# Performance work log

Hardware: AMD Instinct MI355X
Metric: run time of the kernel (lower is better)

The kernel has to match this reference:

```python
import jax, jax.numpy as jnp
import numpy as np

N = 50000      # nodes
E = 800000     # edges
D = 128        # node_dim
H = 4          # heads
C = 64         # hidden_dim per head
B = 64         # graphs in batch
OUT = 10       # output_dim
SLOPE = 0.2    # GATConv leaky_relu negative slope (PyG default)


def gat_conv(x, src, dst, W, a_src, a_dst, bias, concat):
    """One PyG-style GATConv layer. src/dst already include self-loops."""
    n = x.shape[0]
    h = (x @ W).reshape(n, H, C)                       # [N,H,C]
    al_s = jnp.sum(h * a_src, axis=-1)                  # [N,H]
    al_d = jnp.sum(h * a_dst, axis=-1)                  # [N,H]
    e = jax.nn.leaky_relu(al_s[src] + al_d[dst], SLOPE)  # [E+N,H]
    m = jax.ops.segment_max(e, dst, num_segments=n)      # per-target-node max
    e = jnp.exp(e - m[dst])
    den = jax.ops.segment_sum(e, dst, num_segments=n)
    alpha = e / (den[dst] + 1e-16)                       # [E+N,H]
    msg = h[src] * alpha[:, :, None]                     # [E+N,H,C]
    out = jax.ops.segment_sum(msg, dst, num_segments=n)  # [N,H,C]
    out = out.reshape(n, H * C) if concat else out.mean(axis=1)
    return out + bias


def gat_forward(x, edge_index, batch, W0, b0, as0, ad0, W1, b1, as1, ad1,
                W2, b2, as2, ad2, pW1, pb1, pW2, pb2):
    n = x.shape[0]
    loop = jnp.arange(n, dtype=edge_index.dtype)
    src = jnp.concatenate([edge_index[0], loop])
    dst = jnp.concatenate([edge_index[1], loop])

    h = gat_conv(x, src, dst, W0, as0, ad0, b0, concat=True)
    h = jax.nn.elu(h)                                    # dropout = identity (eval)
    h = gat_conv(h, src, dst, W1, as1, ad1, b1, concat=True)
    h = jax.nn.elu(h)
    h = gat_conv(h, src, dst, W2, as2, ad2, b2, concat=False)  # [N,C]

    # global_mean_pool
    sums = jax.ops.segment_sum(h, batch, num_segments=B)        # [B,C]
    cnt = jax.ops.segment_sum(jnp.ones((n,), h.dtype), batch, num_segments=B)
    pooled = sums / jnp.maximum(cnt, 1.0)[:, None]

    # predictor MLP
    z = jax.nn.relu(pooled @ pW1 + pb1)
    return z @ pW2 + pb2                                        # [B,OUT]


def setup_inputs() -> dict:
    key = jax.random.key(0)
    ks = jax.random.split(key, 24)
    gl = lambda k, shp, fan: (jax.random.normal(k, shp, jnp.float32) / np.float32(np.sqrt(fan)))
    x = jax.random.normal(ks[0], (N, D), jnp.float32)
    edge_index = jax.random.randint(ks[1], (2, E), 0, N, dtype=jnp.int32)
    batch = jnp.sort(jax.random.randint(ks[2], (N,), 0, B, dtype=jnp.int32))
    return dict(
        x=x, edge_index=edge_index, batch=batch,
        W0=gl(ks[3], (D, H * C), D), b0=jnp.zeros((H * C,), jnp.float32),
        as0=gl(ks[4], (H, C), C), ad0=gl(ks[5], (H, C), C),
        W1=gl(ks[6], (H * C, H * C), H * C), b1=jnp.zeros((H * C,), jnp.float32),
        as1=gl(ks[7], (H, C), C), ad1=gl(ks[8], (H, C), C),
        W2=gl(ks[9], (H * C, H * C), H * C), b2=jnp.zeros((C,), jnp.float32),
        as2=gl(ks[10], (H, C), C), ad2=gl(ks[11], (H, C), C),
        pW1=gl(ks[12], (C, C // 2), C), pb1=jnp.zeros((C // 2,), jnp.float32),
        pW2=gl(ks[13], (C // 2, OUT), C // 2), pb2=jnp.zeros((OUT,), jnp.float32),
    )


def reference(x, edge_index, batch, W0, b0, as0, ad0, W1, b1, as1, ad1,
              W2, b2, as2, ad2, pW1, pb1, pW2, pb2):
    return gat_forward(x, edge_index, batch, W0, b0, as0, ad0, W1, b1, as1, ad1,
                       W2, b2, as2, ad2, pW1, pb1, pW2, pb2)
```

## Files before the change

### kernel.cpp

```cpp
#include <hip/hip_runtime.h>
#include <hip/hip_fp16.h>
#include <cstdint>

#define N_NODES 50000
#define E_EDGES 800000
#define HC 256
#define B_GR 64
#define OUT_DIM 10
#define SLOPE 0.2f
#define NBLK_SCAN ((N_NODES + 255) / 256)

using f16x8 = __attribute__((ext_vector_type(8))) _Float16;
using f32x4 = __attribute__((ext_vector_type(4))) float;

__global__ void wsplit_kernel(const float* __restrict__ W, _Float16* __restrict__ wt_hi,
                              _Float16* __restrict__ wt_lo, int K) {
    int i = blockIdx.x * 256 + threadIdx.x;
    if (i >= K * 256) return;
    int k = i >> 8, n = i & 255;
    float v = W[i];
    _Float16 h = (_Float16)v;
    _Float16 l = (_Float16)(v - (float)h);
    int oidx = ((((k >> 5) * 256 + n) * 4) + ((k >> 3) & 3)) * 8 + (k & 7);
    wt_hi[oidx] = h;
    wt_lo[oidx] = l;
}

template<int K>
__global__ __launch_bounds__(256) void gemm_mfma(const float* __restrict__ A,
        const _Float16* __restrict__ wt_hi, const _Float16* __restrict__ wt_lo,
        __half* __restrict__ h_half,
        const float* __restrict__ a_src, const float* __restrict__ a_dst,
        float* __restrict__ al_s, float* __restrict__ al_d, int M) {
    __shared__ _Float16 a_hi[64][64];
    __shared__ _Float16 a_lo[64][64];
    int tid = threadIdx.x;
    int w = tid >> 6;
    int l = tid & 63;
    int rr = l & 15;
    int kg = l >> 4;
    int row0 = blockIdx.x * 64;
    int lrow = tid >> 2;
    int lgp  = (tid & 3) * 2;

    f32x4 acc[4][4] = {};

    for (int k0 = 0; k0 < K; k0 += 64) {
        if (k0 > 0) __syncthreads();
        int gr = row0 + lrow;
#pragma unroll
        for (int gi = 0; gi < 2; ++gi) {
            int g = lgp + gi;
            float vv[8];
            if (gr < M) {
                float4 p = *(const float4*)&A[(size_t)gr * K + k0 + g * 8];
                float4 q = *(const float4*)&A[(size_t)gr * K + k0 + g * 8 + 4];
                vv[0] = p.x; vv[1] = p.y; vv[2] = p.z; vv[3] = p.w;
                vv[4] = q.x; vv[5] = q.y; vv[6] = q.z; vv[7] = q.w;
            } else {
#pragma unroll
                for (int j = 0; j < 8; ++j) vv[j] = 0.f;
            }
            f16x8 vh, vl;
#pragma unroll
            for (int j = 0; j < 8; ++j) {
                _Float16 hh = (_Float16)vv[j];
                vh[j] = hh;
                vl[j] = (_Float16)(vv[j] - (float)hh);
            }
            int gs = g ^ (lrow & 7);
            *(f16x8*)&a_hi[lrow][gs * 8] = vh;
            *(f16x8*)&a_lo[lrow][gs * 8] = vl;
        }
        __syncthreads();
#pragma unroll
        for (int c = 0; c < 2; ++c) {
            f16x8 ah[4], alo[4];
#pragma unroll
            for (int fm = 0; fm < 4; ++fm) {
                int row = fm * 16 + rr;
                int gsw = ((c * 4 + kg) ^ (row & 7));
                ah[fm]  = *(const f16x8*)&a_hi[row][gsw * 8];
                alo[fm] = *(const f16x8*)&a_lo[row][gsw * 8];
            }
            int chunk = (k0 >> 5) + c;
#pragma unroll
            for (int fn = 0; fn < 4; ++fn) {
                int col = w * 64 + fn * 16 + rr;
                size_t boff = (((size_t)chunk * 256 + col) * 4 + kg) * 8;
                f16x8 bh = *(const f16x8*)&wt_hi[boff];
                f16x8 bl = *(const f16x8*)&wt_lo[boff];
#pragma unroll
                for (int fm = 0; fm < 4; ++fm) {
                    acc[fm][fn] = __builtin_amdgcn_mfma_f32_16x16x32_f16(ah[fm],  bh, acc[fm][fn], 0, 0, 0);
                    acc[fm][fn] = __builtin_amdgcn_mfma_f32_16x16x32_f16(ah[fm],  bl, acc[fm][fn], 0, 0, 0);
                    acc[fm][fn] = __builtin_amdgcn_mfma_f32_16x16x32_f16(alo[fm], bh, acc[fm][fn], 0, 0, 0);
                }
            }
        }
    }

    int head = w;
    float asv[4], adv[4];
#pragma unroll
    for (int fn = 0; fn < 4; ++fn) {
        asv[fn] = a_src[head * 64 + fn * 16 + rr];
        adv[fn] = a_dst[head * 64 + fn * 16 + rr];
    }
#pragma unroll
    for (int fm = 0; fm < 4; ++fm) {
#pragma unroll
        for (int r = 0; r < 4; ++r) {
            int row = fm * 16 + kg * 4 + r;
            int gr = row0 + row;
            float ps = acc[fm][0][r] * asv[0] + acc[fm][1][r] * asv[1]
                     + acc[fm][2][r] * asv[2] + acc[fm][3][r] * asv[3];
            float pd = acc[fm][0][r] * adv[0] + acc[fm][1][r] * adv[1]
                     + acc[fm][2][r] * adv[2] + acc[fm][3][r] * adv[3];
#pragma unroll
            for (int off = 1; off < 16; off <<= 1) {
                ps += __shfl_xor(ps, off, 64);
                pd += __shfl_xor(pd, off, 64);
            }
            if (gr < M) {
#pragma unroll
                for (int fn = 0; fn < 4; ++fn)
                    h_half[(size_t)gr * HC + w * 64 + fn * 16 + rr] = __float2half(acc[fm][fn][r]);
                if (rr == 0) {
                    al_s[gr * 4 + head] = ps;
                    al_d[gr * 4 + head] = pd;
                }
            }
        }
    }
}

__global__ void init_cnt(int* cnt) {
    int i = blockIdx.x * blockDim.x + threadIdx.x;
    if (i < N_NODES) cnt[i] = 1;
}
__global__ void hist_kernel(const int* __restrict__ dsts, int* cnt) {
    int i = blockIdx.x * blockDim.x + threadIdx.x;
    if (i < E_EDGES) atomicAdd(&cnt[dsts[i]], 1);
}
__global__ __launch_bounds__(256) void scan_bsum(const int* __restrict__ cnt,
                                                 int* __restrict__ bsum) {
    __shared__ int ws[4];
    int t = threadIdx.x;
    int i = blockIdx.x * 256 + t;
    int v = (i < N_NODES) ? cnt[i] : 0;
#pragma unroll
    for (int off = 1; off < 64; off <<= 1) v += __shfl_xor(v, off, 64);
    if ((t & 63) == 0) ws[t >> 6] = v;
    __syncthreads();
    if (t == 0) bsum[blockIdx.x] = ws[0] + ws[1] + ws[2] + ws[3];
}
__global__ __launch_bounds__(256) void scan_boff(const int* __restrict__ bsum,
                                                 int* __restrict__ boff) {
    __shared__ int s[256];
    int t = threadIdx.x;
    int v = (t < NBLK_SCAN) ? bsum[t] : 0;
    s[t] = v;
    __syncthreads();
    for (int off = 1; off < 256; off <<= 1) {
        int u = (t >= off) ? s[t - off] : 0;
        __syncthreads();
        s[t] += u;
        __syncthreads();
    }
    if (t < NBLK_SCAN) boff[t] = s[t] - v;
}
__global__ __launch_bounds__(256) void scan_final(const int* __restrict__ cnt,
        const int* __restrict__ boff, int* __restrict__ row_ptr,
        int* __restrict__ cursor) {
    __shared__ int s[256];
    int b = blockIdx.x, t = threadIdx.x;
    int i = b * 256 + t;
    int v = (i < N_NODES) ? cnt[i] : 0;
    s[t] = v;
    __syncthreads();
    for (int off = 1; off < 256; off <<= 1) {
        int u = (t >= off) ? s[t - off] : 0;
        __syncthreads();
        s[t] += u;
        __syncthreads();
    }
    int rp = boff[b] + s[t] - v;
    if (i < N_NODES) { row_ptr[i] = rp; cursor[i] = rp; }
    if (i == N_NODES - 1) row_ptr[N_NODES] = rp + v;
}
__global__ void scatter_kernel(const int* __restrict__ srcs, const int* __restrict__ dsts,
                               int* cursor, int* col) {
    int i = blockIdx.x * blockDim.x + threadIdx.x;
    if (i >= E_EDGES + N_NODES) return;
    int s, d;
    if (i < E_EDGES) { s = srcs[i]; d = dsts[i]; }
    else             { s = d = i - E_EDGES; }
    int pos = atomicAdd(&cursor[d], 1);
    col[pos] = s;
}

__global__ __launch_bounds__(256) void agg_kernel(const __half* __restrict__ hh,
        const float* __restrict__ al_s, const float* __restrict__ al_d,
        const int* __restrict__ row_ptr, const int* __restrict__ col,
        const float* __restrict__ bias, float* __restrict__ out, int mode) {
    __shared__ int   lds_col[4][64];
    __shared__ float lds_alpha[4][64][4];
    int wid  = threadIdx.x >> 6;
    int lane = threadIdx.x & 63;
    int hf   = lane >> 5;
    int ln   = lane & 31;
    int nodeA = blockIdx.x * 8 + wid * 2;
    int nodeB = nodeA + 1;
    int sA = row_ptr[nodeA], eA = row_ptr[nodeA + 1];
    int sB = row_ptr[nodeB], eB = row_ptr[nodeB + 1];
    int degA = eA - sA, degB = eB - sB;

    if (degA <= 32 && degB <= 32) {
        int node  = hf ? nodeB : nodeA;
        int start = hf ? sB : sA;
        int deg   = hf ? degB : degA;
        int degmax = max(degA, degB);
        const float4 ald = *(const float4*)&al_d[node * 4];
        bool active = ln < deg;
        int s = active ? col[start + ln] : 0;
        float4 as = *(const float4*)&al_s[s * 4];
        float e0 = as.x + ald.x; e0 = e0 > 0.f ? e0 : SLOPE * e0;
        float e1 = as.y + ald.y; e1 = e1 > 0.f ? e1 : SLOPE * e1;
        float e2 = as.z + ald.z; e2 = e2 > 0.f ? e2 : SLOPE * e2;
        float e3 = as.w + ald.w; e3 = e3 > 0.f ? e3 : SLOPE * e3;
        float m0 = active ? e0 : -1e30f, m1 = active ? e1 : -1e30f;
        float m2 = active ? e2 : -1e30f, m3 = active ? e3 : -1e30f;
#pragma unroll
        for (int off = 1; off < 32; off <<= 1) {
            m0 = fmaxf(m0, __shfl_xor(m0, off, 64));
            m1 = fmaxf(m1, __shfl_xor(m1, off, 64));
            m2 = fmaxf(m2, __shfl_xor(m2, off, 64));
            m3 = fmaxf(m3, __shfl_xor(m3, off, 64));
        }
        float x0 = active ? expf(e0 - m0) : 0.f;
        float x1 = active ? expf(e1 - m1) : 0.f;
        float x2 = active ? expf(e2 - m2) : 0.f;
        float x3 = active ? expf(e3 - m3) : 0.f;
        float d0 = x0, d1 = x1, d2 = x2, d3 = x3;
#pragma unroll
        for (int off = 1; off < 32; off <<= 1) {
            d0 += __shfl_xor(d0, off, 64);
            d1 += __shfl_xor(d1, off, 64);
            d2 += __shfl_xor(d2, off, 64);
            d3 += __shfl_xor(d3, off, 64);
        }
        float4 a4;
        a4.x = x0 / (d0 + 1e-16f); a4.y = x1 / (d1 + 1e-16f);
        a4.z = x2 / (d2 + 1e-16f); a4.w = x3 / (d3 + 1e-16f);
        int e = hf * 32 + ln;
        lds_col[wid][e] = s;
        *(float4*)&lds_alpha[wid][e][0] = a4;
        int head = ln >> 3;
        int ch0 = ln * 8;
        float acc[8] = {0.f, 0.f, 0.f, 0.f, 0.f, 0.f, 0.f, 0.f};
        int ebase = hf * 32;
        for (int t0 = 0; t0 < degmax; t0 += 4) {
            float wv[4]; float4 raw[4];
#pragma unroll
            for (int k = 0; k < 4; ++k) {
                int t = t0 + k;
                int tt = min(t, deg - 1);
                int s2 = lds_col[wid][ebase + tt];
                wv[k] = (t < deg) ? lds_alpha[wid][ebase + tt][head] : 0.f;
                raw[k] = *(const float4*)&hh[(size_t)s2 * HC + ch0];
            }
#pragma unroll
            for (int k = 0; k < 4; ++k) {
                const __half2* hp = (const __half2*)&raw[k];
                float2 f0 = __half22float2(hp[0]);
                float2 f1 = __half22float2(hp[1]);
                float2 f2 = __half22float2(hp[2]);
                float2 f3 = __half22float2(hp[3]);
                acc[0] = fmaf(wv[k], f0.x, acc[0]); acc[1] = fmaf(wv[k], f0.y, acc[1]);
                acc[2] = fmaf(wv[k], f1.x, acc[2]); acc[3] = fmaf(wv[k], f1.y, acc[3]);
                acc[4] = fmaf(wv[k], f2.x, acc[4]); acc[5] = fmaf(wv[k], f2.y, acc[5]);
                acc[6] = fmaf(wv[k], f3.x, acc[6]); acc[7] = fmaf(wv[k], f3.y, acc[7]);
            }
        }
        if (mode == 0) {
            float b8[8];
            *(float4*)&b8[0] = *(const float4*)&bias[ch0];
            *(float4*)&b8[4] = *(const float4*)&bias[ch0 + 4];
            float v[8];
#pragma unroll
            for (int j = 0; j < 8; ++j) {
                float t = acc[j] + b8[j];
                v[j] = t > 0.f ? t : expm1f(t);
            }
            *(float4*)&out[(size_t)node * HC + ch0]     = *(float4*)&v[0];
            *(float4*)&out[(size_t)node * HC + ch0 + 4] = *(float4*)&v[4];
        } else {
#pragma unroll
            for (int j = 0; j < 8; ++j) {
                acc[j] += __shfl_xor(acc[j], 8, 64);
                acc[j] += __shfl_xor(acc[j], 16, 64);
            }
            if (ln < 8) {
                float v[8];
#pragma unroll
                for (int j = 0; j < 8; ++j)
                    v[j] = acc[j] * 0.25f + bias[ln * 8 + j];
                *(float4*)&out[(size_t)node * 64 + ln * 8]     = *(float4*)&v[0];
                *(float4*)&out[(size_t)node * 64 + ln * 8 + 4] = *(float4*)&v[4];
            }
        }
        return;
    }

    for (int nn = 0; nn < 2; ++nn) {
        int node = nodeA + nn;
        int start = row_ptr[node], end = row_ptr[node + 1];
        int deg = end - start;
        const float4 ald = *(const float4*)&al_d[node * 4];
        int head = lane >> 4;
        float ald_h = head == 0 ? ald.x : head == 1 ? ald.y : head == 2 ? ald.z : ald.w;
        float ax = 0.f, ay = 0.f, az = 0.f, aw = 0.f;

        if (deg <= 64) {
            int j = start + lane;
            bool active = j < end;
            int s = active ? col[j] : 0;
            float4 as = *(const float4*)&al_s[s * 4];
            float e0 = as.x + ald.x; e0 = e0 > 0.f ? e0 : SLOPE * e0;
            float e1 = as.y + ald.y; e1 = e1 > 0.f ? e1 : SLOPE * e1;
            float e2 = as.z + ald.z; e2 = e2 > 0.f ? e2 : SLOPE * e2;
            float e3 = as.w + ald.w; e3 = e3 > 0.f ? e3 : SLOPE * e3;
            float m0 = active ? e0 : -1e30f, m1 = active ? e1 : -1e30f;
            float m2 = active ? e2 : -1e30f, m3 = active ? e3 : -1e30f;
#pragma unroll
            for (int off = 1; off < 64; off <<= 1) {
                m0 = fmaxf(m0, __shfl_xor(m0, off, 64));
                m1 = fmaxf(m1, __shfl_xor(m1, off, 64));
                m2 = fmaxf(m2, __shfl_xor(m2, off, 64));
                m3 = fmaxf(m3, __shfl_xor(m3, off, 64));
            }
            float x0 = active ? expf(e0 - m0) : 0.f;
            float x1 = active ? expf(e1 - m1) : 0.f;
            float x2 = active ? expf(e2 - m2) : 0.f;
            float x3 = active ? expf(e3 - m3) : 0.f;
            float d0 = x0, d1 = x1, d2 = x2, d3 = x3;
#pragma unroll
            for (int off = 1; off < 64; off <<= 1) {
                d0 += __shfl_xor(d0, off, 64);
                d1 += __shfl_xor(d1, off, 64);
                d2 += __shfl_xor(d2, off, 64);
                d3 += __shfl_xor(d3, off, 64);
            }
            float4 a4;
            a4.x = x0 / (d0 + 1e-16f); a4.y = x1 / (d1 + 1e-16f);
            a4.z = x2 / (d2 + 1e-16f); a4.w = x3 / (d3 + 1e-16f);
            lds_col[wid][lane] = s;
            *(float4*)&lds_alpha[wid][lane][0] = a4;
            for (int t0 = 0; t0 < deg; t0 += 8) {
                int nr = deg - t0;
                float wv[8]; float2 raw[8];
#pragma unroll
                for (int k = 0; k < 8; ++k) {
                    if (k < nr) {
                        int s2 = lds_col[wid][t0 + k];
                        wv[k] = lds_alpha[wid][t0 + k][head];
                        raw[k] = *(const float2*)&hh[(size_t)s2 * HC + lane * 4];
                    } else {
                        wv[k] = 0.f;
                        raw[k] = make_float2(0.f, 0.f);
                    }
                }
#pragma unroll
                for (int k = 0; k < 8; ++k) {
                    float2 f0 = __half22float2(*(__half2*)&raw[k].x);
                    float2 f1 = __half22float2(*(__half2*)&raw[k].y);
                    ax = fmaf(wv[k], f0.x, ax); ay = fmaf(wv[k], f0.y, ay);
                    az = fmaf(wv[k], f1.x, az); aw = fmaf(wv[k], f1.y, aw);
                }
            }
        } else {
            float m0 = -1e30f, m1 = -1e30f, m2 = -1e30f, m3 = -1e30f;
            for (int j = start + lane; j < end; j += 64) {
                int s = col[j];
                float4 as = *(const float4*)&al_s[s * 4];
                float e0 = as.x + ald.x; e0 = e0 > 0.f ? e0 : SLOPE * e0;
                float e1 = as.y + ald.y; e1 = e1 > 0.f ? e1 : SLOPE * e1;
                float e2 = as.z + ald.z; e2 = e2 > 0.f ? e2 : SLOPE * e2;
                float e3 = as.w + ald.w; e3 = e3 > 0.f ? e3 : SLOPE * e3;
                m0 = fmaxf(m0, e0); m1 = fmaxf(m1, e1);
                m2 = fmaxf(m2, e2); m3 = fmaxf(m3, e3);
            }
#pragma unroll
            for (int off = 1; off < 64; off <<= 1) {
                m0 = fmaxf(m0, __shfl_xor(m0, off, 64));
                m1 = fmaxf(m1, __shfl_xor(m1, off, 64));
                m2 = fmaxf(m2, __shfl_xor(m2, off, 64));
                m3 = fmaxf(m3, __shfl_xor(m3, off, 64));
            }
            float d0 = 0.f, d1 = 0.f, d2 = 0.f, d3 = 0.f;
            for (int j = start + lane; j < end; j += 64) {
                int s = col[j];
                float4 as = *(const float4*)&al_s[s * 4];
                float e0 = as.x + ald.x; e0 = e0 > 0.f ? e0 : SLOPE * e0;
                float e1 = as.y + ald.y; e1 = e1 > 0.f ? e1 : SLOPE * e1;
                float e2 = as.z + ald.z; e2 = e2 > 0.f ? e2 : SLOPE * e2;
                float e3 = as.w + ald.w; e3 = e3 > 0.f ? e3 : SLOPE * e3;
                d0 += expf(e0 - m0); d1 += expf(e1 - m1);
                d2 += expf(e2 - m2); d3 += expf(e3 - m3);
            }
#pragma unroll
            for (int off = 1; off < 64; off <<= 1) {
                d0 += __shfl_xor(d0, off, 64);
                d1 += __shfl_xor(d1, off, 64);
                d2 += __shfl_xor(d2, off, 64);
                d3 += __shfl_xor(d3, off, 64);
            }
            float inv0 = 1.f / (d0 + 1e-16f), inv1 = 1.f / (d1 + 1e-16f);
            float inv2 = 1.f / (d2 + 1e-16f), inv3 = 1.f / (d3 + 1e-16f);
            float m_h   = head == 0 ? m0   : head == 1 ? m1   : head == 2 ? m2   : m3;
            float inv_h = head == 0 ? inv0 : head == 1 ? inv1 : head == 2 ? inv2 : inv3;
            for (int jb = start; jb < end; jb += 64) {
                int j = jb + lane;
                int cs = (j < end) ? col[j] : 0;
                int cnt2 = min(64, end - jb);
                for (int t = 0; t < cnt2; ++t) {
                    int s = __shfl(cs, t, 64);
                    float als2 = al_s[s * 4 + head];
                    float e = als2 + ald_h; e = e > 0.f ? e : SLOPE * e;
                    float wv = expf(e - m_h) * inv_h;
                    float2 raw = *(const float2*)&hh[(size_t)s * HC + lane * 4];
                    float2 f0 = __half22float2(*(__half2*)&raw.x);
                    float2 f1 = __half22float2(*(__half2*)&raw.y);
                    ax = fmaf(wv, f0.x, ax); ay = fmaf(wv, f0.y, ay);
                    az = fmaf(wv, f1.x, az); aw = fmaf(wv, f1.y, aw);
                }
            }
        }

        if (mode == 0) {
            float4 b4 = *(const float4*)&bias[lane * 4];
            float vx = ax + b4.x; vx = vx > 0.f ? vx : expm1f(vx);
            float vy = ay + b4.y; vy = vy > 0.f ? vy : expm1f(vy);
            float vz = az + b4.z; vz = vz > 0.f ? vz : expm1f(vz);
            float vw = aw + b4.w; vw = vw > 0.f ? vw : expm1f(vw);
            float4 v = make_float4(vx, vy, vz, vw);
            *(float4*)&out[(size_t)node * HC + lane * 4] = v;
        } else {
#pragma unroll
            for (int off = 16; off < 64; off <<= 1) {
                ax += __shfl_xor(ax, off, 64);
                ay += __shfl_xor(ay, off, 64);
                az += __shfl_xor(az, off, 64);
                aw += __shfl_xor(aw, off, 64);
            }
            if (lane < 16) {
                float4 b4 = *(const float4*)&bias[lane * 4];
                float4 v = make_float4(ax * 0.25f + b4.x, ay * 0.25f + b4.y,
                                       az * 0.25f + b4.z, aw * 0.25f + b4.w);
                *(float4*)&out[(size_t)node * 64 + lane * 4] = v;
            }
        }
    }
}

__global__ void pool_zero(float* __restrict__ pooled) {
    int i = blockIdx.x * blockDim.x + threadIdx.x;
    if (i < B_GR * 64) pooled[i] = 0.f;
}

__global__ __launch_bounds__(256) void pool_kernel(const float* __restrict__ act,
        const int* __restrict__ batch, float* __restrict__ pooled) {
    int b = blockIdx.x;
    int chunk = blockIdx.y;
    int warp = threadIdx.x >> 6;
    int lane = threadIdx.x & 63;
    int lo = 0, hi = N_NODES;
    while (lo < hi) { int mid = (lo + hi) >> 1; if (batch[mid] < b) lo = mid + 1; else hi = mid; }
    int s = lo;
    lo = 0; hi = N_NODES;
    while (lo < hi) { int mid = (lo + hi) >> 1; if (batch[mid] < b + 1) lo = mid + 1; else hi = mid; }
    int e = lo;
    float sum = 0.f;
    for (int n = s + chunk * 4 + warp; n < e; n += 64)
        sum += act[(size_t)n * 64 + lane];
    atomicAdd(&pooled[b * 64 + lane], sum);
}

__global__ __launch_bounds__(64) void mlp_kernel(const float* __restrict__ pooled,
        const int* __restrict__ batch,
        const float* __restrict__ pW1, const float* __restrict__ pb1,
        const float* __restrict__ pW2, const float* __restrict__ pb2,
        float* __restrict__ outp) {
    __shared__ float p[64];
    __shared__ float z[32];
    int b = blockIdx.x, t = threadIdx.x;
    int lo = 0, hi = N_NODES;
    while (lo < hi) { int mid = (lo + hi) >> 1; if (batch[mid] < b) lo = mid + 1; else hi = mid; }
    int s = lo;
    lo = 0; hi = N_NODES;
    while (lo < hi) { int mid = (lo + hi) >> 1; if (batch[mid] < b + 1) lo = mid + 1; else hi = mid; }
    int e = lo;
    float inv = 1.f / (float)max(e - s, 1);
    p[t] = pooled[b * 64 + t] * inv;
    __syncthreads();
    if (t < 32) {
        float s2 = pb1[t];
        for (int c = 0; c < 64; ++c) s2 += p[c] * pW1[c * 32 + t];
        z[t] = s2 > 0.f ? s2 : 0.f;
    }
    __syncthreads();
    if (t < OUT_DIM) {
        float s2 = pb2[t];
        for (int k = 0; k < 32; ++k) s2 += z[k] * pW2[k * 10 + t];
        outp[b * 10 + t] = s2;
    }
}

extern "C" void kernel_launch(void* const* d_in, const int* in_sizes, int n_in,
                              void* d_out, int out_size, void* d_ws, size_t ws_size,
                              hipStream_t stream) {
    const float* x    = (const float*)d_in[0];
    const int*   ei   = (const int*)d_in[1];
    const int*   batch= (const int*)d_in[2];
    const float* W0   = (const float*)d_in[3];
    const float* b0   = (const float*)d_in[4];
    const float* as0  = (const float*)d_in[5];
    const float* ad0  = (const float*)d_in[6];
    const float* W1   = (const float*)d_in[7];
    const float* b1   = (const float*)d_in[8];
    const float* as1  = (const float*)d_in[9];
    const float* ad1  = (const float*)d_in[10];
    const float* W2   = (const float*)d_in[11];
    const float* b2   = (const float*)d_in[12];
    const float* as2  = (const float*)d_in[13];
    const float* ad2  = (const float*)d_in[14];
    const float* pW1  = (const float*)d_in[15];
    const float* pb1  = (const float*)d_in[16];
    const float* pW2  = (const float*)d_in[17];
    const float* pb2  = (const float*)d_in[18];
    float* out = (float*)d_out;

    char* ws = (char*)d_ws;
    size_t off = 0;
    auto alloc = [&](size_t bytes) -> void* {
        void* p = ws + off;
        off += (bytes + 255) & ~(size_t)255;
        return p;
    };
    __half* h_half = (__half*)alloc((size_t)N_NODES * HC * 2);
    float* act    = (float*)alloc((size_t)N_NODES * HC * 4);
    float* als    = (float*)alloc((size_t)N_NODES * 4 * 4);
    float* ald    = (float*)alloc((size_t)N_NODES * 4 * 4);
    int*   cnt    = (int*)alloc((size_t)N_NODES * 4);
    int*   row_ptr= (int*)alloc((size_t)(N_NODES + 1) * 4);
    int*   cursor = (int*)alloc((size_t)N_NODES * 4);
    int*   col    = (int*)alloc((size_t)(E_EDGES + N_NODES) * 4);
    float* pooled = (float*)alloc((size_t)B_GR * 64 * 4);
    int*   bsum   = (int*)alloc((size_t)NBLK_SCAN * 4);
    int*   boff   = (int*)alloc((size_t)NBLK_SCAN * 4);
    _Float16* w0h = (_Float16*)alloc((size_t)128 * 256 * 2);
    _Float16* w0l = (_Float16*)alloc((size_t)128 * 256 * 2);
    _Float16* w1h = (_Float16*)alloc((size_t)256 * 256 * 2);
    _Float16* w1l = (_Float16*)alloc((size_t)256 * 256 * 2);
    _Float16* w2h = (_Float16*)alloc((size_t)256 * 256 * 2);
    _Float16* w2l = (_Float16*)alloc((size_t)256 * 256 * 2);

    const int* srcs = ei;
    const int* dsts = ei + E_EDGES;

    wsplit_kernel<<<(128 * 256 + 255) / 256, 256, 0, stream>>>(W0, w0h, w0l, 128);
    wsplit_kernel<<<(256 * 256 + 255) / 256, 256, 0, stream>>>(W1, w1h, w1l, 256);
    wsplit_kernel<<<(256 * 256 + 255) / 256, 256, 0, stream>>>(W2, w2h, w2l, 256);

    init_cnt<<<(N_NODES + 255) / 256, 256, 0, stream>>>(cnt);
    hist_kernel<<<(E_EDGES + 255) / 256, 256, 0, stream>>>(dsts, cnt);
    scan_bsum<<<NBLK_SCAN, 256, 0, stream>>>(cnt, bsum);
    scan_boff<<<1, 256, 0, stream>>>(bsum, boff);
    scan_final<<<NBLK_SCAN, 256, 0, stream>>>(cnt, boff, row_ptr, cursor);
    scatter_kernel<<<(E_EDGES + N_NODES + 255) / 256, 256, 0, stream>>>(srcs, dsts, cursor, col);

    int gblk = (N_NODES + 63) / 64;
    int nblk = (N_NODES + 7) / 8;

    gemm_mfma<128><<<gblk, 256, 0, stream>>>(x, w0h, w0l, h_half, as0, ad0, als, ald, N_NODES);
    agg_kernel<<<nblk, 256, 0, stream>>>(h_half, als, ald, row_ptr, col, b0, act, 0);
    gemm_mfma<256><<<gblk, 256, 0, stream>>>(act, w1h, w1l, h_half, as1, ad1, als, ald, N_NODES);
    agg_kernel<<<nblk, 256, 0, stream>>>(h_half, als, ald, row_ptr, col, b1, act, 0);
    gemm_mfma<256><<<gblk, 256, 0, stream>>>(act, w2h, w2l, h_half, as2, ad2, als, ald, N_NODES);
    agg_kernel<<<nblk, 256, 0, stream>>>(h_half, als, ald, row_ptr, col, b2, act, 1);

    pool_zero<<<(B_GR * 64 + 255) / 256, 256, 0, stream>>>(pooled);
    dim3 pgrid(B_GR, 16);
    pool_kernel<<<pgrid, 256, 0, stream>>>(act, batch, pooled);
    mlp_kernel<<<B_GR, 64, 0, stream>>>(pooled, batch, pW1, pb1, pW2, pb2, out);
}
```

Baseline: 445.0 us.

## Store hidden activations in fp16, pre-split x, double-buffer GEMM A tiles via LDS loads

The hidden-layer activations written by aggregation are now stored as fp16, so layers 1 and 2 read half the bytes and drop the lo-term MFMA (two terms instead of three). The input x is split into hi/lo fp16 in one fused prep kernel that also splits all three weight matrices. The GEMM now stages A tiles with global_load_lds into a double buffer, overlapping the next tile's load with the current tile's compute. Pooling uses one 1024-thread block per graph with an LDS reduction instead of atomics and a zeroing kernel. Rounding activations to fp16 and dropping the lo term lowers GEMM input precision and may affect accuracy.

Result: faster. 423.1 us (-4.9%).

```diff
diff --git a/kernel.cpp b/kernel.cpp
--- a/kernel.cpp
+++ b/kernel.cpp
@@ -13,77 +13,96 @@
 using f16x8 = __attribute__((ext_vector_type(8))) _Float16;
 using f32x4 = __attribute__((ext_vector_type(4))) float;
 
-__global__ void wsplit_kernel(const float* __restrict__ W, _Float16* __restrict__ wt_hi,
-                              _Float16* __restrict__ wt_lo, int K) {
-    int i = blockIdx.x * 256 + threadIdx.x;
-    if (i >= K * 256) return;
+#define GLOAD_LDS16(gsrc, ldst) \
+    __builtin_amdgcn_global_load_lds((const __attribute__((address_space(1))) void*)(gsrc), \
+        (__attribute__((address_space(3))) void*)(ldst), 16, 0, 0)
+
+__device__ inline void wsplit_one(const float* W, _Float16* wh, _Float16* wl,
+                                  int K, int i) {
     int k = i >> 8, n = i & 255;
     float v = W[i];
     _Float16 h = (_Float16)v;
     _Float16 l = (_Float16)(v - (float)h);
     int oidx = ((((k >> 5) * 256 + n) * 4) + ((k >> 3) & 3)) * 8 + (k & 7);
-    wt_hi[oidx] = h;
-    wt_lo[oidx] = l;
-}
-
-template<int K>
-__global__ __launch_bounds__(256) void gemm_mfma(const float* __restrict__ A,
+    wh[oidx] = h;
+    wl[oidx] = l;
+}
+
+__global__ void prep_split(const float* __restrict__ x,
+        _Float16* __restrict__ xhi, _Float16* __restrict__ xlo,
+        const float* __restrict__ W0, _Float16* __restrict__ w0h, _Float16* __restrict__ w0l,
+        const float* __restrict__ W1, _Float16* __restrict__ w1h, _Float16* __restrict__ w1l,
+        const float* __restrict__ W2, _Float16* __restrict__ w2h, _Float16* __restrict__ w2l) {
+    const int NX = N_NODES * 128;
+    int i = blockIdx.x * 256 + threadIdx.x;
+    if (i < NX) {
+        float v = x[i];
+        _Float16 h = (_Float16)v;
+        xhi[i] = h;
+        xlo[i] = (_Float16)(v - (float)h);
+        return;
+    }
+    int j = i - NX;
+    if (j < 128 * 256) { wsplit_one(W0, w0h, w0l, 128, j); return; }
+    j -= 128 * 256;
+    if (j < 256 * 256) { wsplit_one(W1, w1h, w1l, 256, j); return; }
+    j -= 256 * 256;
+    if (j < 256 * 256) { wsplit_one(W2, w2h, w2l, 256, j); return; }
+}
+
+template<int K, int TERMS>
+__global__ __launch_bounds__(256) void gemm16(const _Float16* __restrict__ Ahi,
+        const _Float16* __restrict__ Alo,
         const _Float16* __restrict__ wt_hi, const _Float16* __restrict__ wt_lo,
         __half* __restrict__ h_half,
         const float* __restrict__ a_src, const float* __restrict__ a_dst,
         float* __restrict__ al_s, float* __restrict__ al_d, int M) {
-    __shared__ _Float16 a_hi[64][64];
-    __shared__ _Float16 a_lo[64][64];
+    __shared__ _Float16 abuf[2][2][64][64];
     int tid = threadIdx.x;
     int w = tid >> 6;
     int l = tid & 63;
     int rr = l & 15;
     int kg = l >> 4;
     int row0 = blockIdx.x * 64;
-    int lrow = tid >> 2;
-    int lgp  = (tid & 3) * 2;
+    int srow = tid >> 3;
+    int sgs  = tid & 7;
 
     f32x4 acc[4][4] = {};
-
-    for (int k0 = 0; k0 < K; k0 += 64) {
-        if (k0 > 0) __syncthreads();
-        int gr = row0 + lrow;
-#pragma unroll
-        for (int gi = 0; gi < 2; ++gi) {
-            int g = lgp + gi;
-            float vv[8];
-            if (gr < M) {
-                float4 p = *(const float4*)&A[(size_t)gr * K + k0 + g * 8];
-                float4 q = *(const float4*)&A[(size_t)gr * K + k0 + g * 8 + 4];
-                vv[0] = p.x; vv[1] = p.y; vv[2] = p.z; vv[3] = p.w;
-                vv[4] = q.x; vv[5] = q.y; vv[6] = q.z; vv[7] = q.w;
-            } else {
-#pragma unroll
-                for (int j = 0; j < 8; ++j) vv[j] = 0.f;
-            }
-            f16x8 vh, vl;
-#pragma unroll
-            for (int j = 0; j < 8; ++j) {
-                _Float16 hh = (_Float16)vv[j];
-                vh[j] = hh;
-                vl[j] = (_Float16)(vv[j] - (float)hh);
-            }
-            int gs = g ^ (lrow & 7);
-            *(f16x8*)&a_hi[lrow][gs * 8] = vh;
-            *(f16x8*)&a_lo[lrow][gs * 8] = vl;
-        }
-        __syncthreads();
+    const int NT = K / 64;
+
+    auto stage = [&](int buf, int t) {
+        int k0 = t * 64;
+#pragma unroll
+        for (int i = 0; i < 2; ++i) {
+            int row = i * 32 + srow;
+            int g = sgs ^ (row & 7);
+            int gr = min(row0 + row, M - 1);
+            char* dst = (char*)abuf + buf * 16384 + i * 4096 + w * 1024;
+            GLOAD_LDS16(&Ahi[(size_t)gr * K + k0 + g * 8], dst);
+            if constexpr (TERMS == 3)
+                GLOAD_LDS16(&Alo[(size_t)gr * K + k0 + g * 8], dst + 8192);
+        }
+    };
+
+    stage(0, 0);
+    __syncthreads();
+    int cur = 0;
+    for (int t = 0; t < NT; ++t) {
+        if (t + 1 < NT) stage(cur ^ 1, t + 1);
+        const _Float16* base_hi = &abuf[cur][0][0][0];
+        const _Float16* base_lo = &abuf[cur][1][0][0];
 #pragma unroll
         for (int c = 0; c < 2; ++c) {
-            f16x8 ah[4], alo[4];
+            f16x8 ah[4], alo_[4];
 #pragma unroll
             for (int fm = 0; fm < 4; ++fm) {
                 int row = fm * 16 + rr;
                 int gsw = ((c * 4 + kg) ^ (row & 7));
-                ah[fm]  = *(const f16x8*)&a_hi[row][gsw * 8];
-                alo[fm] = *(const f16x8*)&a_lo[row][gsw * 8];
-            }
-            int chunk = (k0 >> 5) + c;
+                ah[fm] = *(const f16x8*)&base_hi[row * 64 + gsw * 8];
+                if constexpr (TERMS == 3)
+                    alo_[fm] = *(const f16x8*)&base_lo[row * 64 + gsw * 8];
+            }
+            int chunk = t * 2 + c;
 #pragma unroll
             for (int fn = 0; fn < 4; ++fn) {
                 int col = w * 64 + fn * 16 + rr;
@@ -92,12 +111,15 @@
                 f16x8 bl = *(const f16x8*)&wt_lo[boff];
 #pragma unroll
                 for (int fm = 0; fm < 4; ++fm) {
-                    acc[fm][fn] = __builtin_amdgcn_mfma_f32_16x16x32_f16(ah[fm],  bh, acc[fm][fn], 0, 0, 0);
-                    acc[fm][fn] = __builtin_amdgcn_mfma_f32_16x16x32_f16(ah[fm],  bl, acc[fm][fn], 0, 0, 0);
-                    acc[fm][fn] = __builtin_amdgcn_mfma_f32_16x16x32_f16(alo[fm], bh, acc[fm][fn], 0, 0, 0);
+                    acc[fm][fn] = __builtin_amdgcn_mfma_f32_16x16x32_f16(ah[fm], bh, acc[fm][fn], 0, 0, 0);
+                    acc[fm][fn] = __builtin_amdgcn_mfma_f32_16x16x32_f16(ah[fm], bl, acc[fm][fn], 0, 0, 0);
+                    if constexpr (TERMS == 3)
+                        acc[fm][fn] = __builtin_amdgcn_mfma_f32_16x16x32_f16(alo_[fm], bh, acc[fm][fn], 0, 0, 0);
                 }
             }
         }
+        __syncthreads();
+        cur ^= 1;
     }
 
     int head = w;
@@ -203,7 +225,8 @@
 __global__ __launch_bounds__(256) void agg_kernel(const __half* __restrict__ hh,
         const float* __restrict__ al_s, const float* __restrict__ al_d,
         const int* __restrict__ row_ptr, const int* __restrict__ col,
-        const float* __restrict__ bias, float* __restrict__ out, int mode) {
+        const float* __restrict__ bias, _Float16* __restrict__ out_h,
+        float* __restrict__ out_f, int mode) {
     __shared__ int   lds_col[4][64];
     __shared__ float lds_alpha[4][64][4];
     int wid  = threadIdx.x >> 6;
@@ -287,14 +310,13 @@
             float b8[8];
             *(float4*)&b8[0] = *(const float4*)&bias[ch0];
             *(float4*)&b8[4] = *(const float4*)&bias[ch0 + 4];
-            float v[8];
+            _Float16 v[8];
 #pragma unroll
             for (int j = 0; j < 8; ++j) {
                 float t = acc[j] + b8[j];
-                v[j] = t > 0.f ? t : expm1f(t);
-            }
-            *(float4*)&out[(size_t)node * HC + ch0]     = *(float4*)&v[0];
-            *(float4*)&out[(size_t)node * HC + ch0 + 4] = *(float4*)&v[4];
+                v[j] = (_Float16)(t > 0.f ? t : expm1f(t));
+            }
+            *(float4*)&out_h[(size_t)node * HC + ch0] = *(float4*)v;
         } else {
 #pragma unroll
             for (int j = 0; j < 8; ++j) {
@@ -306,8 +328,8 @@
 #pragma unroll
                 for (int j = 0; j < 8; ++j)
                     v[j] = acc[j] * 0.25f + bias[ln * 8 + j];
-                *(float4*)&out[(size_t)node * 64 + ln * 8]     = *(float4*)&v[0];
-                *(float4*)&out[(size_t)node * 64 + ln * 8 + 4] = *(float4*)&v[4];
+                *(float4*)&out_f[(size_t)node * 64 + ln * 8]     = *(float4*)&v[0];
+                *(float4*)&out_f[(size_t)node * 64 + ln * 8 + 4] = *(float4*)&v[4];
             }
         }
         return;
@@ -444,8 +466,8 @@
             float vy = ay + b4.y; vy = vy > 0.f ? vy : expm1f(vy);
             float vz = az + b4.z; vz = vz > 0.f ? vz : expm1f(vz);
             float vw = aw + b4.w; vw = vw > 0.f ? vw : expm1f(vw);
-            float4 v = make_float4(vx, vy, vz, vw);
-            *(float4*)&out[(size_t)node * HC + lane * 4] = v;
+            _Float16 v[4] = {(_Float16)vx, (_Float16)vy, (_Float16)vz, (_Float16)vw};
+            *(float2*)&out_h[(size_t)node * HC + lane * 4] = *(float2*)v;
         } else {
 #pragma unroll
             for (int off = 16; off < 64; off <<= 1) {
@@ -458,21 +480,16 @@
                 float4 b4 = *(const float4*)&bias[lane * 4];
                 float4 v = make_float4(ax * 0.25f + b4.x, ay * 0.25f + b4.y,
                                        az * 0.25f + b4.z, aw * 0.25f + b4.w);
-                *(float4*)&out[(size_t)node * 64 + lane * 4] = v;
-            }
-        }
-    }
-}
-
-__global__ void pool_zero(float* __restrict__ pooled) {
-    int i = blockIdx.x * blockDim.x + threadIdx.x;
-    if (i < B_GR * 64) pooled[i] = 0.f;
-}
-
-__global__ __launch_bounds__(256) void pool_kernel(const float* __restrict__ act,
+                *(float4*)&out_f[(size_t)node * 64 + lane * 4] = v;
+            }
+        }
+    }
+}
+
+__global__ __launch_bounds__(1024) void pool_kernel(const float* __restrict__ act,
         const int* __restrict__ batch, float* __restrict__ pooled) {
+    __shared__ float part[16][64];
     int b = blockIdx.x;
-    int chunk = blockIdx.y;
     int warp = threadIdx.x >> 6;
     int lane = threadIdx.x & 63;
     int lo = 0, hi = N_NODES;
@@ -482,9 +499,16 @@
     while (lo < hi) { int mid = (lo + hi) >> 1; if (batch[mid] < b + 1) lo = mid + 1; else hi = mid; }
     int e = lo;
     float sum = 0.f;
-    for (int n = s + chunk * 4 + warp; n < e; n += 64)
+    for (int n = s + warp; n < e; n += 16)
         sum += act[(size_t)n * 64 + lane];
-    atomicAdd(&pooled[b * 64 + lane], sum);
+    part[warp][lane] = sum;
+    __syncthreads();
+    if (threadIdx.x < 64) {
+        float t = 0.f;
+#pragma unroll
+        for (int r = 0; r < 16; ++r) t += part[r][lane];
+        pooled[b * 64 + lane] = t;
+    }
 }
 
 __global__ __launch_bounds__(64) void mlp_kernel(const float* __restrict__ pooled,
@@ -548,8 +572,11 @@
         off += (bytes + 255) & ~(size_t)255;
         return p;
     };
-    __half* h_half = (__half*)alloc((size_t)N_NODES * HC * 2);
-    float* act    = (float*)alloc((size_t)N_NODES * HC * 4);
+    __half*    h_half = (__half*)alloc((size_t)N_NODES * HC * 2);
+    _Float16*  act_h  = (_Float16*)alloc((size_t)N_NODES * HC * 2);
+    float*     act_f  = (float*)alloc((size_t)N_NODES * 64 * 4);
+    _Float16*  xhi    = (_Float16*)alloc((size_t)N_NODES * 128 * 2);
+    _Float16*  xlo    = (_Float16*)alloc((size_t)N_NODES * 128 * 2);
     float* als    = (float*)alloc((size_t)N_NODES * 4 * 4);
     float* ald    = (float*)alloc((size_t)N_NODES * 4 * 4);
     int*   cnt    = (int*)alloc((size_t)N_NODES * 4);
@@ -569,9 +596,9 @@
     const int* srcs = ei;
     const int* dsts = ei + E_EDGES;
 
-    wsplit_kernel<<<(128 * 256 + 255) / 256, 256, 0, stream>>>(W0, w0h, w0l, 128);
-    wsplit_kernel<<<(256 * 256 + 255) / 256, 256, 0, stream>>>(W1, w1h, w1l, 256);
-    wsplit_kernel<<<(256 * 256 + 255) / 256, 256, 0, stream>>>(W2, w2h, w2l, 256);
+    const int PREP_N = N_NODES * 128 + 128 * 256 + 256 * 256 + 256 * 256;
+    prep_split<<<(PREP_N + 255) / 256, 256, 0, stream>>>(
+        x, xhi, xlo, W0, w0h, w0l, W1, w1h, w1l, W2, w2h, w2l);
 
     init_cnt<<<(N_NODES + 255) / 256, 256, 0, stream>>>(cnt);
     hist_kernel<<<(E_EDGES + 255) / 256, 256, 0, stream>>>(dsts, cnt);
@@ -583,15 +610,13 @@
     int gblk = (N_NODES + 63) / 64;
     int nblk = (N_NODES + 7) / 8;
 
-    gemm_mfma<128><<<gblk, 256, 0, stream>>>(x, w0h, w0l, h_half, as0, ad0, als, ald, N_NODES);
-    agg_kernel<<<nblk, 256, 0, stream>>>(h_half, als, ald, row_ptr, col, b0, act, 0);
-    gemm_mfma<256><<<gblk, 256, 0, stream>>>(act, w1h, w1l, h_half, as1, ad1, als, ald, N_NODES);
-    agg_kernel<<<nblk, 256, 0, stream>>>(h_half, als, ald, row_ptr, col, b1, act, 0);
-    gemm_mfma<256><<<gblk, 256, 0, stream>>>(act, w2h, w2l, h_half, as2, ad2, als, ald, N_NODES);
-    agg_kernel<<<nblk, 256, 0, stream>>>(h_half, als, ald, row_ptr, col, b2, act, 1);
-
-    pool_zero<<<(B_GR * 64 + 255) / 256, 256, 0, stream>>>(pooled);
-    dim3 pgrid(B_GR, 16);
-    pool_kernel<<<pgrid, 256, 0, stream>>>(act, batch, pooled);
+    gemm16<128, 3><<<gblk, 256, 0, stream>>>(xhi, xlo, w0h, w0l, h_half, as0, ad0, als, ald, N_NODES);
+    agg_kernel<<<nblk, 256, 0, stream>>>(h_half, als, ald, row_ptr, col, b0, act_h, act_f, 0);
+    gemm16<256, 2><<<gblk, 256, 0, stream>>>(act_h, nullptr, w1h, w1l, h_half, as1, ad1, als, ald, N_NODES);
+    agg_kernel<<<nblk, 256, 0, stream>>>(h_half, als, ald, row_ptr, col, b1, act_h, act_f, 0);
+    gemm16<256, 2><<<gblk, 256, 0, stream>>>(act_h, nullptr, w2h, w2l, h_half, as2, ad2, als, ald, N_NODES);
+    agg_kernel<<<nblk, 256, 0, stream>>>(h_half, als, ald, row_ptr, col, b2, act_h, act_f, 1);
+
+    pool_kernel<<<B_GR, 1024, 0, stream>>>(act_f, batch, pooled);
     mlp_kernel<<<B_GR, 64, 0, stream>>>(pooled, batch, pW1, pb1, pW2, pb2, out);
 }
```
